# Performance work log

Measured on AMD Instinct MI355X. Metric: run time of the kernel, lower is better.

Reference implementation:

```python
import jax, jax.numpy as jnp
import numpy as np

N_NODES = 1024
NUM_MOL = 32
ATOMS = 32          # atoms per molecule
SDIM = 256
VDIM = 64
EDIM = 128
NUM_BOND_TYPES = 5


def _fully_connected_edges():
    # all ordered pairs (j, i), j != i, within each molecule block
    idx = np.arange(ATOMS)
    jj, ii = np.meshgrid(idx, idx, indexing='ij')
    mask = jj != ii
    jj, ii = jj[mask], ii[mask]                      # [ATOMS*(ATOMS-1)]
    offs = (np.arange(NUM_MOL) * ATOMS)[:, None]
    j_all = (jj[None, :] + offs).reshape(-1)
    i_all = (ii[None, :] + offs).reshape(-1)
    return np.stack([j_all, i_all]).astype(np.int32)  # [2, E]


def setup_inputs() -> dict:
    key = jax.random.key(0)
    ks = jax.random.split(key, 12)
    edge_index = jnp.asarray(_fully_connected_edges())  # [2, 31744]
    E = edge_index.shape[1]
    inp = {
        's': jax.random.normal(ks[0], (N_NODES, SDIM), jnp.float32),
        'v': jax.random.normal(ks[1], (N_NODES, 3, VDIM), jnp.float32),
        'p': jax.random.normal(ks[2], (N_NODES, 3), jnp.float32),
        'e': jax.random.normal(ks[3], (E, EDIM), jnp.float32),
        'batch': jnp.repeat(jnp.arange(NUM_MOL, dtype=jnp.int32), ATOMS),
        'edge_index': edge_index,
        # learned parameters
        'W_shared': jax.random.normal(ks[4], (SDIM, SDIM), jnp.float32) * 0.02,
        'b_shared': jnp.zeros((SDIM,), jnp.float32),
        'W_coords': jax.random.normal(ks[5], (VDIM, 1), jnp.float32) * 0.02,
        'W_bond': jax.random.normal(ks[6], (EDIM, SDIM), jnp.float32) * 0.02,
        'b_bond': jnp.zeros((SDIM,), jnp.float32),
        'W_b0': jax.random.normal(ks[7], (SDIM + 1, SDIM), jnp.float32) * 0.02,
        'b_b0': jnp.zeros((SDIM,), jnp.float32),
        'W_b1': jax.random.normal(ks[8], (SDIM, NUM_BOND_TYPES), jnp.float32) * 0.02,
        'b_b1': jnp.zeros((NUM_BOND_TYPES,), jnp.float32),
    }
    return inp


def reference(s, v, p, e, batch, edge_index,
              W_shared, b_shared, W_coords, W_bond, b_bond,
              W_b0, b_b0, W_b1, b_b1):
    n = s.shape[0]
    # shared_mapping: DenseLayer with SiLU
    s = jax.nn.silu(s @ W_shared + b_shared)
    # coords_lin: [n,3,vdim] @ [vdim,1] -> [n,3]
    coords = p + jnp.einsum('ncv,vo->nc', v, W_coords)
    # scatter_mean centering per molecule
    seg_sum = jax.ops.segment_sum(coords, batch, num_segments=NUM_MOL)
    counts = jax.ops.segment_sum(jnp.ones((n, 1), coords.dtype), batch,
                                 num_segments=NUM_MOL)
    mean = seg_sum / jnp.maximum(counts, 1.0)
    coords = coords - mean[batch]
    # dense symmetrization of edge features
    j, i = edge_index[0], edge_index[1]
    e_dense = jnp.zeros((n, n, e.shape[-1]), e.dtype).at[j, i].set(e)
    e_dense = 0.5 * (e_dense + jnp.swapaxes(e_dense, 0, 1))
    e_sym = e_dense[j, i]                                  # [E, EDIM]
    # squared distance per edge
    d = jnp.sum((coords[i] - coords[j]) ** 2, axis=-1, keepdims=True)  # [E,1]
    # edge MLP
    f = s[i] + s[j] + (e_sym @ W_bond + b_bond)            # [E, SDIM]
    edge = jnp.concatenate([f, d], axis=-1)                # [E, SDIM+1]
    h = jax.nn.silu(edge @ W_b0 + b_b0)
    bonds_pred = h @ W_b1 + b_b1                           # [E, 5]
    return bonds_pred
```

## Files before the change

### kernel.cpp

```cpp
#include <hip/hip_runtime.h>
#include <hip/hip_bf16.h>

#define N_NODES 1024
#define NUM_MOL 32
#define ATOMS 32
#define SDIM 256
#define VDIM 64
#define EDIM 128
#define NBT 5
#define EDGES_PER_MOL (ATOMS * (ATOMS - 1))
#define PAIRS_PER_MOL (ATOMS * (ATOMS - 1) / 2)
#define N_PAIRS (NUM_MOL * PAIRS_PER_MOL)

typedef __attribute__((ext_vector_type(8))) short bf16x8;
typedef __attribute__((ext_vector_type(4))) float f32x4;

__device__ __forceinline__ unsigned short f2bf(float x) {
    union { float f; unsigned int u; } v; v.f = x;
    unsigned int r = v.u + 0x7fffu + ((v.u >> 16) & 1u);
    return (unsigned short)(r >> 16);
}

__device__ __forceinline__ bf16x8 pack8(const float4& x0, const float4& x1) {
    bf16x8 r;
    r[0] = (short)f2bf(x0.x); r[1] = (short)f2bf(x0.y);
    r[2] = (short)f2bf(x0.z); r[3] = (short)f2bf(x0.w);
    r[4] = (short)f2bf(x1.x); r[5] = (short)f2bf(x1.y);
    r[6] = (short)f2bf(x1.z); r[7] = (short)f2bf(x1.w);
    return r;
}

__global__ __launch_bounds__(256) void prep_kernel(
    const float* __restrict__ Ws, const float* __restrict__ Wb0,
    unsigned short* __restrict__ Wsf, unsigned short* __restrict__ Wb0f)
{
    const int t   = threadIdx.x;
    const int bid = blockIdx.x;
    const float* W = (bid < 32) ? Ws : Wb0;
    unsigned short* dst = (bid < 32) ? Wsf : Wb0f;
    const int g    = ((bid & 31) << 8) + t;
    const int lane = g & 63;
    const int kt   = (g >> 6) & 7;
    const int nt   = g >> 9;
    const int n     = nt * 16 + (lane & 15);
    const int kbase = kt * 32 + (lane >> 4) * 8;
    const float* col = W + (size_t)kbase * SDIM + n;
    bf16x8 r;
#pragma unroll
    for (int e2 = 0; e2 < 8; ++e2) r[e2] = (short)f2bf(col[(size_t)e2 * SDIM]);
    *(bf16x8*)&dst[(size_t)g * 8] = r;
}

__global__ __launch_bounds__(256) void node_kernel(
    const float* __restrict__ s,
    const unsigned short* __restrict__ Wsf,
    const unsigned short* __restrict__ Wb0f,
    const float* __restrict__ bs,
    const float* __restrict__ Wbond, const float* __restrict__ bbond,
    const float* __restrict__ Wb0, const float* __restrict__ bb0,
    const float* __restrict__ v, const float* __restrict__ p,
    const float* __restrict__ Wc,
    float* __restrict__ sp2, unsigned short* __restrict__ Wf,
    float* __restrict__ coords, float* __restrict__ bcomb)
{
    __shared__ __align__(16) unsigned short s2u[16 * 256];
    const int t = threadIdx.x;
    const int bid = blockIdx.x;
    const int w = t >> 6, l = t & 63;
    const int kg = l >> 4, lr = l & 15;

    if (bid < 64) {
        const int r0 = bid * 16;

        bf16x8 a[8];
        const float* srow = s + (size_t)(r0 + lr) * SDIM + kg * 8;
#pragma unroll
        for (int kt = 0; kt < 8; ++kt) {
            const float4 x0 = *(const float4*)(srow + kt * 32);
            const float4 x1 = *(const float4*)(srow + kt * 32 + 4);
            a[kt] = pack8(x0, x1);
        }

        const bf16x8* wsp = (const bf16x8*)Wsf;
        f32x4 acc[4];
#pragma unroll
        for (int q = 0; q < 4; ++q) {
            acc[q][0] = 0.f; acc[q][1] = 0.f; acc[q][2] = 0.f; acc[q][3] = 0.f;
            const int nt = w * 4 + q;
#pragma unroll
            for (int kt = 0; kt < 8; ++kt) {
                const bf16x8 bf = wsp[(nt * 8 + kt) * 64 + l];
                acc[q] = __builtin_amdgcn_mfma_f32_16x16x32_bf16(a[kt], bf, acc[q], 0, 0, 0);
            }
        }

#pragma unroll
        for (int q = 0; q < 4; ++q) {
            const int n = (w * 4 + q) * 16 + lr;
            const float bsv = bs[n];
#pragma unroll
            for (int j = 0; j < 4; ++j) {
                const int row = kg * 4 + j;
                const float x = acc[q][j] + bsv;
                const float sl = x / (1.f + __expf(-x));
                s2u[(row * 256 + n) ^ ((row & 7) << 3)] = f2bf(sl);
            }
        }
        __syncthreads();

#pragma unroll
        for (int kt = 0; kt < 8; ++kt) {
            const int idx = (lr * 256 + kt * 32 + kg * 8) ^ ((lr & 7) << 3);
            a[kt] = *(const bf16x8*)&s2u[idx];
        }

        const bf16x8* wbp = (const bf16x8*)Wb0f;
#pragma unroll
        for (int q = 0; q < 4; ++q) {
            acc[q][0] = 0.f; acc[q][1] = 0.f; acc[q][2] = 0.f; acc[q][3] = 0.f;
            const int nt = w * 4 + q;
#pragma unroll
            for (int kt = 0; kt < 8; ++kt) {
                const bf16x8 bf = wbp[(nt * 8 + kt) * 64 + l];
                acc[q] = __builtin_amdgcn_mfma_f32_16x16x32_bf16(a[kt], bf, acc[q], 0, 0, 0);
            }
        }
#pragma unroll
        for (int q = 0; q < 4; ++q) {
            const int n = (w * 4 + q) * 16 + lr;
#pragma unroll
            for (int j = 0; j < 4; ++j)
                sp2[(size_t)(r0 + kg * 4 + j) * SDIM + n] = acc[q][j];
        }

    } else if (bid < 72) {
        const int r0 = (bid - 64) * 16;

        bf16x8 a[8];
        const float* wrow = Wbond + (size_t)(r0 + lr) * SDIM + kg * 8;
#pragma unroll
        for (int kt = 0; kt < 8; ++kt) {
            const float4 x0 = *(const float4*)(wrow + kt * 32);
            const float4 x1 = *(const float4*)(wrow + kt * 32 + 4);
            a[kt] = pack8(x0, x1);
        }

        const bf16x8* wbp = (const bf16x8*)Wb0f;
        f32x4 acc[4];
#pragma unroll
        for (int q = 0; q < 4; ++q) {
            acc[q][0] = 0.f; acc[q][1] = 0.f; acc[q][2] = 0.f; acc[q][3] = 0.f;
            const int nt = w * 4 + q;
#pragma unroll
            for (int kt = 0; kt < 8; ++kt) {
                const bf16x8 bf = wbp[(nt * 8 + kt) * 64 + l];
                acc[q] = __builtin_amdgcn_mfma_f32_16x16x32_bf16(a[kt], bf, acc[q], 0, 0, 0);
            }
        }

#pragma unroll
        for (int q = 0; q < 4; ++q) {
            const int nt2 = w * 4 + q;
#pragma unroll
            for (int j = 0; j < 4; ++j) {
                const int krow = r0 + kg * 4 + j;
                const int kt2 = krow >> 5, g2 = (krow >> 3) & 3, eidx = krow & 7;
                const int lane2 = lr + 16 * g2;
                Wf[((size_t)((nt2 * 4 + kt2) * 64 + lane2)) * 8 + eidx] =
                    f2bf(0.5f * acc[q][j]);
            }
        }

    } else if (bid < 104) {
        const int mol = bid - 72;
        float* cl   = (float*)s2u;
        float* mean = (float*)s2u + 100;
        if (t < ATOMS * 3) {
            const int a = t / 3, dim = t % 3;
            const int node = mol * ATOMS + a;
            const float* vv = v + (size_t)node * 3 * VDIM + dim * VDIM;
            float acc = 0.f;
#pragma unroll 8
            for (int k = 0; k < VDIM; ++k) acc += vv[k] * Wc[k];
            cl[a * 3 + dim] = p[node * 3 + dim] + acc;
        }
        __syncthreads();
        if (t < 3) {
            float sum = 0.f;
            for (int a = 0; a < ATOMS; ++a) sum += cl[a * 3 + t];
            mean[t] = sum * (1.f / ATOMS);
        }
        __syncthreads();
        if (t < ATOMS * 3) {
            const int a = t / 3, dim = t % 3;
            coords[(mol * ATOMS + a) * 3 + dim] = cl[a * 3 + dim] - mean[dim];
        }
    } else {
        float acc = bb0[t];
#pragma unroll 16
        for (int m = 0; m < SDIM; ++m) acc += bbond[m] * Wb0[m * SDIM + t];
        bcomb[t] = acc;
    }
}

#define PB 16
__global__ __launch_bounds__(256) void edge_mfma_kernel(
    const float* __restrict__ sp2, const float* __restrict__ coords,
    const float* __restrict__ e, const unsigned short* __restrict__ Wf,
    const float* __restrict__ bcomb, const float* __restrict__ Wb0,
    const float* __restrict__ Wb1, const float* __restrict__ bb1,
    float* __restrict__ out)
{
    __shared__ __align__(16) float spsum[PB][260];
    __shared__ __align__(16) unsigned short esym[PB * EDIM];
    __shared__ float wb1s[SDIM * NBT];
    __shared__ float bb1s[8];
    __shared__ int   ksh[PB], krevsh[PB], ish[PB], jsh[PB];
    __shared__ float dsh[PB];

    const int t = threadIdx.x;
    const int bid = (blockIdx.x & 7) * 124 + (blockIdx.x >> 3);
    const int P0  = bid * PB;

    for (int idx = t; idx < SDIM * NBT; idx += 256) wb1s[idx] = Wb1[idx];
    if (t < NBT) bb1s[t] = bb1[t];
    if (t < PB) {
        const int P   = P0 + t;
        const int mol = P / PAIRS_PER_MOL;
        const int p   = P - mol * PAIRS_PER_MOL;
        int jj = (int)((63.0f - sqrtf((float)(3969 - 8 * p))) * 0.5f);
        if (jj < 0) jj = 0;
        if (jj > 30) jj = 30;
        while (jj > 0 && (63 * jj - jj * jj) / 2 > p) --jj;
        while (jj < 30 && (63 * (jj + 1) - (jj + 1) * (jj + 1)) / 2 <= p) ++jj;
        const int Ojj = (63 * jj - jj * jj) / 2;
        const int ii  = jj + 1 + (p - Ojj);
        const int q    = jj * 31 + (ii - 1);
        const int qrev = ii * 31 + jj;
        ksh[t]    = mol * EDGES_PER_MOL + q;
        krevsh[t] = mol * EDGES_PER_MOL + qrev;
        const int i = mol * ATOMS + ii, j = mol * ATOMS + jj;
        ish[t] = i; jsh[t] = j;
        const float dx = coords[i * 3 + 0] - coords[j * 3 + 0];
        const float dy = coords[i * 3 + 1] - coords[j * 3 + 1];
        const float dz = coords[i * 3 + 2] - coords[j * 3 + 2];
        dsh[t] = dx * dx + dy * dy + dz * dz;
    }
    __syncthreads();

    {
        const int r  = t >> 4;
        const int c8 = (t & 15) * 8;
        const float* ek  = e + (size_t)ksh[r] * EDIM + c8;
        const float* ekr = e + (size_t)krevsh[r] * EDIM + c8;
        const float4 x0 = *(const float4*)(ek);
        const float4 x1 = *(const float4*)(ek + 4);
        const float4 y0 = *(const float4*)(ekr);
        const float4 y1 = *(const float4*)(ekr + 4);

        const int c0 = (t & 15) * 4;
        const float* ai = sp2 + (size_t)ish[r] * SDIM;
        const float* aj = sp2 + (size_t)jsh[r] * SDIM;
        const float* w2 = Wb0 + (size_t)SDIM * SDIM;
        const float d = dsh[r];
#pragma unroll
        for (int i = 0; i < 4; ++i) {
            const int c = c0 + 64 * i;
            const float4 a4 = *(const float4*)(ai + c);
            const float4 b4 = *(const float4*)(aj + c);
            const float4 w4 = *(const float4*)(w2 + c);
            const float4 g4 = *(const float4*)(bcomb + c);
            float4 rv;
            rv.x = a4.x + b4.x + d * w4.x + g4.x;
            rv.y = a4.y + b4.y + d * w4.y + g4.y;
            rv.z = a4.z + b4.z + d * w4.z + g4.z;
            rv.w = a4.w + b4.w + d * w4.w + g4.w;
            *(float4*)&spsum[r][c] = rv;
        }

        float4 sx, sy;
        sx.x = x0.x + y0.x; sx.y = x0.y + y0.y; sx.z = x0.z + y0.z; sx.w = x0.w + y0.w;
        sy.x = x1.x + y1.x; sy.y = x1.y + y1.y; sy.z = x1.z + y1.z; sy.w = x1.w + y1.w;
        const int idx = (r * EDIM + c8) ^ ((r & 7) << 3);
        *(bf16x8*)&esym[idx] = pack8(sx, sy);
    }
    __syncthreads();

    const int w = t >> 6, l = t & 63;
    const int kg = l >> 4, lr = l & 15;

    bf16x8 afrag[4];
#pragma unroll
    for (int kt = 0; kt < 4; ++kt) {
        const int idx = (lr * EDIM + kt * 32 + kg * 8) ^ ((lr & 7) << 3);
        afrag[kt] = *(const bf16x8*)&esym[idx];
    }

    const bf16x8* wfp = (const bf16x8*)Wf;
    f32x4 acc[4];
#pragma unroll
    for (int q = 0; q < 4; ++q) {
        acc[q][0] = 0.f; acc[q][1] = 0.f; acc[q][2] = 0.f; acc[q][3] = 0.f;
        const int nt = w * 4 + q;
        const bf16x8 b0 = wfp[(nt * 4 + 0) * 64 + l];
        const bf16x8 b1 = wfp[(nt * 4 + 1) * 64 + l];
        const bf16x8 b2 = wfp[(nt * 4 + 2) * 64 + l];
        const bf16x8 b3 = wfp[(nt * 4 + 3) * 64 + l];
        acc[q] = __builtin_amdgcn_mfma_f32_16x16x32_bf16(afrag[0], b0, acc[q], 0, 0, 0);
        acc[q] = __builtin_amdgcn_mfma_f32_16x16x32_bf16(afrag[1], b1, acc[q], 0, 0, 0);
        acc[q] = __builtin_amdgcn_mfma_f32_16x16x32_bf16(afrag[2], b2, acc[q], 0, 0, 0);
        acc[q] = __builtin_amdgcn_mfma_f32_16x16x32_bf16(afrag[3], b3, acc[q], 0, 0, 0);
    }

#pragma unroll
    for (int q = 0; q < 4; ++q) {
        const int n = (w * 4 + q) * 16 + lr;
#pragma unroll
        for (int j = 0; j < 4; ++j) {
            const int r = kg * 4 + j;
            const float x = acc[q][j] + spsum[r][n];
            spsum[r][n] = x / (1.f + __expf(-x));
        }
    }
    __syncthreads();

    if (t < PB * NBT * 2) {
        const int task = t >> 1, half = t & 1;
        const int r  = task / NBT;
        const int tt = task - r * NBT;
        float a = half ? 0.f : bb1s[tt];
        const int base = half * 32;
#pragma unroll 4
        for (int cc = 0; cc < 32; ++cc) {
            const int c4 = base + ((cc + task) & 31);
            const int c  = c4 * 4;
            const float4 hv = *(const float4*)&spsum[r][c];
            a += hv.x * wb1s[(c + 0) * NBT + tt] + hv.y * wb1s[(c + 1) * NBT + tt] +
                 hv.z * wb1s[(c + 2) * NBT + tt] + hv.w * wb1s[(c + 3) * NBT + tt];
        }
        a += __shfl_xor(a, 1);
        if (!half) {
            out[(size_t)ksh[r] * NBT + tt]    = a;
            out[(size_t)krevsh[r] * NBT + tt] = a;
        }
    }
}

extern "C" void kernel_launch(void* const* d_in, const int* in_sizes, int n_in,
                              void* d_out, int out_size, void* d_ws, size_t ws_size,
                              hipStream_t stream)
{
    const float* s        = (const float*)d_in[0];
    const float* v        = (const float*)d_in[1];
    const float* p        = (const float*)d_in[2];
    const float* e        = (const float*)d_in[3];
    const float* W_shared = (const float*)d_in[6];
    const float* b_shared = (const float*)d_in[7];
    const float* W_coords = (const float*)d_in[8];
    const float* W_bond   = (const float*)d_in[9];
    const float* b_bond   = (const float*)d_in[10];
    const float* W_b0     = (const float*)d_in[11];
    const float* b_b0     = (const float*)d_in[12];
    const float* W_b1     = (const float*)d_in[13];
    const float* b_b1     = (const float*)d_in[14];
    float* out = (float*)d_out;

    char* ws = (char*)d_ws;
    float*          sp2    = (float*)(ws + 0);
    unsigned short* Wsf    = (unsigned short*)(ws + 1048576);
    unsigned short* Wb0f   = (unsigned short*)(ws + 1179648);
    unsigned short* Wf     = (unsigned short*)(ws + 1310720);
    float*          bcomb  = (float*)(ws + 1376256);
    float*          coords = (float*)(ws + 1377280);

    prep_kernel<<<64, 256, 0, stream>>>(W_shared, W_b0, Wsf, Wb0f);
    node_kernel<<<105, 256, 0, stream>>>(s, Wsf, Wb0f, b_shared,
                                         W_bond, b_bond, W_b0, b_b0,
                                         v, p, W_coords,
                                         sp2, Wf, coords, bcomb);
    edge_mfma_kernel<<<N_PAIRS / PB, 256, 0, stream>>>(sp2, coords, e, Wf, bcomb,
                                                       W_b0, W_b1, b_b1, out);
}
```

Measured before the change: 28.12 us.

## Compute pair indices per thread, drop sync, prefetch MFMA weights before barrier

Every thread now computes its pair's edge indices and squared distance directly, so the first barrier and the serial 16-thread index stage are gone. The Wb1 staging is vectorised and moved after the gathers, and half of the bf16 weight fragments for the MFMA are prefetched into registers before the barrier to overlap global latency. The final projection loop gets two accumulators to shorten dependency chains. The cost is redundant index math in every thread and higher register pressure from the prefetched fragments.

```diff
diff --git a/kernel.cpp b/kernel.cpp
--- a/kernel.cpp
+++ b/kernel.cpp
@@ -213,59 +213,51 @@
 {
     __shared__ __align__(16) float spsum[PB][260];
     __shared__ __align__(16) unsigned short esym[PB * EDIM];
-    __shared__ float wb1s[SDIM * NBT];
+    __shared__ __align__(16) float wb1s[SDIM * NBT];
     __shared__ float bb1s[8];
-    __shared__ int   ksh[PB], krevsh[PB], ish[PB], jsh[PB];
-    __shared__ float dsh[PB];
+    __shared__ int   ksh[PB], krevsh[PB];
 
     const int t = threadIdx.x;
     const int bid = (blockIdx.x & 7) * 124 + (blockIdx.x >> 3);
     const int P0  = bid * PB;
 
-    for (int idx = t; idx < SDIM * NBT; idx += 256) wb1s[idx] = Wb1[idx];
-    if (t < NBT) bb1s[t] = bb1[t];
-    if (t < PB) {
-        const int P   = P0 + t;
-        const int mol = P / PAIRS_PER_MOL;
-        const int p   = P - mol * PAIRS_PER_MOL;
-        int jj = (int)((63.0f - sqrtf((float)(3969 - 8 * p))) * 0.5f);
-        if (jj < 0) jj = 0;
-        if (jj > 30) jj = 30;
-        while (jj > 0 && (63 * jj - jj * jj) / 2 > p) --jj;
-        while (jj < 30 && (63 * (jj + 1) - (jj + 1) * (jj + 1)) / 2 <= p) ++jj;
-        const int Ojj = (63 * jj - jj * jj) / 2;
-        const int ii  = jj + 1 + (p - Ojj);
-        const int q    = jj * 31 + (ii - 1);
-        const int qrev = ii * 31 + jj;
-        ksh[t]    = mol * EDGES_PER_MOL + q;
-        krevsh[t] = mol * EDGES_PER_MOL + qrev;
-        const int i = mol * ATOMS + ii, j = mol * ATOMS + jj;
-        ish[t] = i; jsh[t] = j;
-        const float dx = coords[i * 3 + 0] - coords[j * 3 + 0];
-        const float dy = coords[i * 3 + 1] - coords[j * 3 + 1];
-        const float dz = coords[i * 3 + 2] - coords[j * 3 + 2];
-        dsh[t] = dx * dx + dy * dy + dz * dz;
-    }
-    __syncthreads();
+    const int r   = t >> 4;
+    const int P   = P0 + r;
+    const int mol = P / PAIRS_PER_MOL;
+    const int p   = P - mol * PAIRS_PER_MOL;
+    int jj = (int)((63.0f - sqrtf((float)(3969 - 8 * p))) * 0.5f);
+    if (jj < 0) jj = 0;
+    if (jj > 30) jj = 30;
+    while (jj > 0 && (63 * jj - jj * jj) / 2 > p) --jj;
+    while (jj < 30 && (63 * (jj + 1) - (jj + 1) * (jj + 1)) / 2 <= p) ++jj;
+    const int Ojj  = (63 * jj - jj * jj) / 2;
+    const int ii   = jj + 1 + (p - Ojj);
+    const int k    = mol * EDGES_PER_MOL + jj * 31 + (ii - 1);
+    const int krev = mol * EDGES_PER_MOL + ii * 31 + jj;
+    const int i = mol * ATOMS + ii, j = mol * ATOMS + jj;
+    if ((t & 15) == 0) { ksh[r] = k; krevsh[r] = krev; }
+
+    const int c8 = (t & 15) * 8;
+    const float* ek  = e + (size_t)k * EDIM + c8;
+    const float* ekr = e + (size_t)krev * EDIM + c8;
+    const float4 x0 = *(const float4*)(ek);
+    const float4 x1 = *(const float4*)(ek + 4);
+    const float4 y0 = *(const float4*)(ekr);
+    const float4 y1 = *(const float4*)(ekr + 4);
+
+    const float dx = coords[i * 3 + 0] - coords[j * 3 + 0];
+    const float dy = coords[i * 3 + 1] - coords[j * 3 + 1];
+    const float dz = coords[i * 3 + 2] - coords[j * 3 + 2];
+    const float d  = dx * dx + dy * dy + dz * dz;
 
     {
-        const int r  = t >> 4;
-        const int c8 = (t & 15) * 8;
-        const float* ek  = e + (size_t)ksh[r] * EDIM + c8;
-        const float* ekr = e + (size_t)krevsh[r] * EDIM + c8;
-        const float4 x0 = *(const float4*)(ek);
-        const float4 x1 = *(const float4*)(ek + 4);
-        const float4 y0 = *(const float4*)(ekr);
-        const float4 y1 = *(const float4*)(ekr + 4);
-
         const int c0 = (t & 15) * 4;
-        const float* ai = sp2 + (size_t)ish[r] * SDIM;
-        const float* aj = sp2 + (size_t)jsh[r] * SDIM;
+        const float* ai = sp2 + (size_t)i * SDIM;
+        const float* aj = sp2 + (size_t)j * SDIM;
         const float* w2 = Wb0 + (size_t)SDIM * SDIM;
-        const float d = dsh[r];
-#pragma unroll
-        for (int i = 0; i < 4; ++i) {
-            const int c = c0 + 64 * i;
+#pragma unroll
+        for (int it = 0; it < 4; ++it) {
+            const int c = c0 + 64 * it;
             const float4 a4 = *(const float4*)(ai + c);
             const float4 b4 = *(const float4*)(aj + c);
             const float4 w4 = *(const float4*)(w2 + c);
@@ -277,17 +269,31 @@
             rv.w = a4.w + b4.w + d * w4.w + g4.w;
             *(float4*)&spsum[r][c] = rv;
         }
-
+    }
+
+    {
         float4 sx, sy;
         sx.x = x0.x + y0.x; sx.y = x0.y + y0.y; sx.z = x0.z + y0.z; sx.w = x0.w + y0.w;
         sy.x = x1.x + y1.x; sy.y = x1.y + y1.y; sy.z = x1.z + y1.z; sy.w = x1.w + y1.w;
         const int idx = (r * EDIM + c8) ^ ((r & 7) << 3);
         *(bf16x8*)&esym[idx] = pack8(sx, sy);
     }
-    __syncthreads();
+
+    for (int idx4 = t; idx4 < SDIM * NBT / 4; idx4 += 256)
+        *(float4*)&wb1s[idx4 * 4] = *(const float4*)&Wb1[idx4 * 4];
+    if (t < NBT) bb1s[t] = bb1[t];
 
     const int w = t >> 6, l = t & 63;
     const int kg = l >> 4, lr = l & 15;
+    const bf16x8* wfp = (const bf16x8*)Wf;
+    bf16x8 bpre[8];
+#pragma unroll
+    for (int q = 0; q < 2; ++q)
+#pragma unroll
+        for (int kt = 0; kt < 4; ++kt)
+            bpre[q * 4 + kt] = wfp[((w * 4 + q) * 4 + kt) * 64 + l];
+
+    __syncthreads();
 
     bf16x8 afrag[4];
 #pragma unroll
@@ -296,10 +302,17 @@
         afrag[kt] = *(const bf16x8*)&esym[idx];
     }
 
-    const bf16x8* wfp = (const bf16x8*)Wf;
     f32x4 acc[4];
 #pragma unroll
-    for (int q = 0; q < 4; ++q) {
+    for (int q = 0; q < 2; ++q) {
+        acc[q][0] = 0.f; acc[q][1] = 0.f; acc[q][2] = 0.f; acc[q][3] = 0.f;
+        acc[q] = __builtin_amdgcn_mfma_f32_16x16x32_bf16(afrag[0], bpre[q * 4 + 0], acc[q], 0, 0, 0);
+        acc[q] = __builtin_amdgcn_mfma_f32_16x16x32_bf16(afrag[1], bpre[q * 4 + 1], acc[q], 0, 0, 0);
+        acc[q] = __builtin_amdgcn_mfma_f32_16x16x32_bf16(afrag[2], bpre[q * 4 + 2], acc[q], 0, 0, 0);
+        acc[q] = __builtin_amdgcn_mfma_f32_16x16x32_bf16(afrag[3], bpre[q * 4 + 3], acc[q], 0, 0, 0);
+    }
+#pragma unroll
+    for (int q = 2; q < 4; ++q) {
         acc[q][0] = 0.f; acc[q][1] = 0.f; acc[q][2] = 0.f; acc[q][3] = 0.f;
         const int nt = w * 4 + q;
         const bf16x8 b0 = wfp[(nt * 4 + 0) * 64 + l];
@@ -316,32 +329,37 @@
     for (int q = 0; q < 4; ++q) {
         const int n = (w * 4 + q) * 16 + lr;
 #pragma unroll
-        for (int j = 0; j < 4; ++j) {
-            const int r = kg * 4 + j;
-            const float x = acc[q][j] + spsum[r][n];
-            spsum[r][n] = x / (1.f + __expf(-x));
+        for (int jt = 0; jt < 4; ++jt) {
+            const int rr = kg * 4 + jt;
+            const float x = acc[q][jt] + spsum[rr][n];
+            spsum[rr][n] = x / (1.f + __expf(-x));
         }
     }
     __syncthreads();
 
     if (t < PB * NBT * 2) {
         const int task = t >> 1, half = t & 1;
-        const int r  = task / NBT;
-        const int tt = task - r * NBT;
-        float a = half ? 0.f : bb1s[tt];
+        const int rr = task / NBT;
+        const int tt = task - rr * NBT;
+        float a0 = half ? 0.f : bb1s[tt];
+        float a1 = 0.f;
         const int base = half * 32;
 #pragma unroll 4
-        for (int cc = 0; cc < 32; ++cc) {
-            const int c4 = base + ((cc + task) & 31);
-            const int c  = c4 * 4;
-            const float4 hv = *(const float4*)&spsum[r][c];
-            a += hv.x * wb1s[(c + 0) * NBT + tt] + hv.y * wb1s[(c + 1) * NBT + tt] +
-                 hv.z * wb1s[(c + 2) * NBT + tt] + hv.w * wb1s[(c + 3) * NBT + tt];
-        }
+        for (int cc = 0; cc < 32; cc += 2) {
+            const int ca = (base + ((cc + task) & 31)) * 4;
+            const int cb = (base + ((cc + 1 + task) & 31)) * 4;
+            const float4 hva = *(const float4*)&spsum[rr][ca];
+            const float4 hvb = *(const float4*)&spsum[rr][cb];
+            a0 += hva.x * wb1s[(ca + 0) * NBT + tt] + hva.y * wb1s[(ca + 1) * NBT + tt] +
+                  hva.z * wb1s[(ca + 2) * NBT + tt] + hva.w * wb1s[(ca + 3) * NBT + tt];
+            a1 += hvb.x * wb1s[(cb + 0) * NBT + tt] + hvb.y * wb1s[(cb + 1) * NBT + tt] +
+                  hvb.z * wb1s[(cb + 2) * NBT + tt] + hvb.w * wb1s[(cb + 3) * NBT + tt];
+        }
+        float a = a0 + a1;
         a += __shfl_xor(a, 1);
         if (!half) {
-            out[(size_t)ksh[r] * NBT + tt]    = a;
-            out[(size_t)krevsh[r] * NBT + tt] = a;
+            out[(size_t)ksh[rr] * NBT + tt]    = a;
+            out[(size_t)krevsh[rr] * NBT + tt] = a;
         }
     }
 }
```

After: 28.66 us. No clear change (+2.0%).

## Fuse weight prep into node kernel via LDS-staged fp32 weight chunks

Applied to the files above, without the earlier changes.

Drops the separate prep kernel that converted W_shared and W_b0 into MFMA-swizzled bf16 layouts. Each GEMM block now streams 32-row fp32 chunks of the weight into LDS with register double-buffering, then converts to bf16 per lane while reading the B operand. This saves one kernel launch and the extra global round trip for the packed weights. In exchange every block re-reads and re-converts the full weight matrices, adds many barriers, and uses more LDS.

```diff
diff --git a/kernel.cpp b/kernel.cpp
--- a/kernel.cpp
+++ b/kernel.cpp
@@ -30,32 +30,16 @@
     return r;
 }
 
-__global__ __launch_bounds__(256) void prep_kernel(
-    const float* __restrict__ Ws, const float* __restrict__ Wb0,
-    unsigned short* __restrict__ Wsf, unsigned short* __restrict__ Wb0f)
-{
-    const int t   = threadIdx.x;
-    const int bid = blockIdx.x;
-    const float* W = (bid < 32) ? Ws : Wb0;
-    unsigned short* dst = (bid < 32) ? Wsf : Wb0f;
-    const int g    = ((bid & 31) << 8) + t;
-    const int lane = g & 63;
-    const int kt   = (g >> 6) & 7;
-    const int nt   = g >> 9;
-    const int n     = nt * 16 + (lane & 15);
-    const int kbase = kt * 32 + (lane >> 4) * 8;
-    const float* col = W + (size_t)kbase * SDIM + n;
-    bf16x8 r;
-#pragma unroll
-    for (int e2 = 0; e2 < 8; ++e2) r[e2] = (short)f2bf(col[(size_t)e2 * SDIM]);
-    *(bf16x8*)&dst[(size_t)g * 8] = r;
-}
-
-__global__ __launch_bounds__(256) void node_kernel(
+#define CHS 258
+
+struct PreSm {
+    float chunk[32][CHS];
+    unsigned short s2u[16 * 256];
+};
+
+__global__ __launch_bounds__(256) void pre_kernel(
     const float* __restrict__ s,
-    const unsigned short* __restrict__ Wsf,
-    const unsigned short* __restrict__ Wb0f,
-    const float* __restrict__ bs,
+    const float* __restrict__ Ws, const float* __restrict__ bs,
     const float* __restrict__ Wbond, const float* __restrict__ bbond,
     const float* __restrict__ Wb0, const float* __restrict__ bb0,
     const float* __restrict__ v, const float* __restrict__ p,
@@ -63,35 +47,81 @@
     float* __restrict__ sp2, unsigned short* __restrict__ Wf,
     float* __restrict__ coords, float* __restrict__ bcomb)
 {
-    __shared__ __align__(16) unsigned short s2u[16 * 256];
+    __shared__ __align__(16) char smem[sizeof(PreSm)];
+    PreSm* sm = (PreSm*)smem;
     const int t = threadIdx.x;
     const int bid = blockIdx.x;
     const int w = t >> 6, l = t & 63;
     const int kg = l >> 4, lr = l & 15;
 
-    if (bid < 64) {
-        const int r0 = bid * 16;
+    if (bid < 72) {
+        const bool isnode = (bid < 64);
+        const int r0 = isnode ? bid * 16 : (bid - 64) * 16;
 
         bf16x8 a[8];
-        const float* srow = s + (size_t)(r0 + lr) * SDIM + kg * 8;
+        {
+            const float* arow = (isnode ? s : Wbond) + (size_t)(r0 + lr) * SDIM + kg * 8;
+#pragma unroll
+            for (int kt = 0; kt < 8; ++kt) {
+                const float4 x0 = *(const float4*)(arow + kt * 32);
+                const float4 x1 = *(const float4*)(arow + kt * 32 + 4);
+                a[kt] = pack8(x0, x1);
+            }
+        }
+
+        f32x4 acc[4];
+        float4 stg[8];
+        const float* Wg1 = isnode ? Ws : Wb0;
+
+#pragma unroll
+        for (int i = 0; i < 8; ++i) {
+            const int idx = t + 256 * i, row = idx >> 6, c4 = idx & 63;
+            stg[i] = *(const float4*)&Wg1[(size_t)row * SDIM + c4 * 4];
+        }
+#pragma unroll
+        for (int q = 0; q < 4; ++q) { acc[q][0]=0.f; acc[q][1]=0.f; acc[q][2]=0.f; acc[q][3]=0.f; }
+
 #pragma unroll
         for (int kt = 0; kt < 8; ++kt) {
-            const float4 x0 = *(const float4*)(srow + kt * 32);
-            const float4 x1 = *(const float4*)(srow + kt * 32 + 4);
-            a[kt] = pack8(x0, x1);
-        }
-
-        const bf16x8* wsp = (const bf16x8*)Wsf;
-        f32x4 acc[4];
-#pragma unroll
-        for (int q = 0; q < 4; ++q) {
-            acc[q][0] = 0.f; acc[q][1] = 0.f; acc[q][2] = 0.f; acc[q][3] = 0.f;
-            const int nt = w * 4 + q;
-#pragma unroll
-            for (int kt = 0; kt < 8; ++kt) {
-                const bf16x8 bf = wsp[(nt * 8 + kt) * 64 + l];
+#pragma unroll
+            for (int i = 0; i < 8; ++i) {
+                const int idx = t + 256 * i, row = idx >> 6, c4 = idx & 63;
+                *(float4*)&sm->chunk[row][c4 * 4] = stg[i];
+            }
+            __syncthreads();
+            if (kt < 7) {
+                const float* wsrc = Wg1 + (size_t)((kt + 1) * 32) * SDIM;
+#pragma unroll
+                for (int i = 0; i < 8; ++i) {
+                    const int idx = t + 256 * i, row = idx >> 6, c4 = idx & 63;
+                    stg[i] = *(const float4*)&wsrc[(size_t)row * SDIM + c4 * 4];
+                }
+            }
+#pragma unroll
+            for (int q = 0; q < 4; ++q) {
+                const int n = (w * 4 + q) * 16 + lr;
+                bf16x8 bf;
+#pragma unroll
+                for (int e2 = 0; e2 < 8; ++e2) bf[e2] = (short)f2bf(sm->chunk[kg * 8 + e2][n]);
                 acc[q] = __builtin_amdgcn_mfma_f32_16x16x32_bf16(a[kt], bf, acc[q], 0, 0, 0);
             }
+            __syncthreads();
+        }
+
+        if (!isnode) {
+#pragma unroll
+            for (int q = 0; q < 4; ++q) {
+                const int nt2 = w * 4 + q;
+#pragma unroll
+                for (int j = 0; j < 4; ++j) {
+                    const int krow = r0 + kg * 4 + j;
+                    const int kt2 = krow >> 5, g2 = (krow >> 3) & 3, eidx = krow & 7;
+                    const int lane2 = lr + 16 * g2;
+                    Wf[((size_t)((nt2 * 4 + kt2) * 64 + lane2)) * 8 + eidx] =
+                        f2bf(0.5f * acc[q][j]);
+                }
+            }
+            return;
         }
 
 #pragma unroll
@@ -103,7 +133,7 @@
                 const int row = kg * 4 + j;
                 const float x = acc[q][j] + bsv;
                 const float sl = x / (1.f + __expf(-x));
-                s2u[(row * 256 + n) ^ ((row & 7) << 3)] = f2bf(sl);
+                sm->s2u[(row * 256 + n) ^ ((row & 7) << 3)] = f2bf(sl);
             }
         }
         __syncthreads();
@@ -111,17 +141,40 @@
 #pragma unroll
         for (int kt = 0; kt < 8; ++kt) {
             const int idx = (lr * 256 + kt * 32 + kg * 8) ^ ((lr & 7) << 3);
-            a[kt] = *(const bf16x8*)&s2u[idx];
-        }
-
-        const bf16x8* wbp = (const bf16x8*)Wb0f;
-#pragma unroll
-        for (int q = 0; q < 4; ++q) {
-            acc[q][0] = 0.f; acc[q][1] = 0.f; acc[q][2] = 0.f; acc[q][3] = 0.f;
-            const int nt = w * 4 + q;
-#pragma unroll
-            for (int kt = 0; kt < 8; ++kt) {
-                const bf16x8 bf = wbp[(nt * 8 + kt) * 64 + l];
+            a[kt] = *(const bf16x8*)&sm->s2u[idx];
+        }
+
+#pragma unroll
+        for (int i = 0; i < 8; ++i) {
+            const int idx = t + 256 * i, row = idx >> 6, c4 = idx & 63;
+            stg[i] = *(const float4*)&Wb0[(size_t)row * SDIM + c4 * 4];
+        }
+#pragma unroll
+        for (int q = 0; q < 4; ++q) { acc[q][0]=0.f; acc[q][1]=0.f; acc[q][2]=0.f; acc[q][3]=0.f; }
+
+#pragma unroll
+        for (int kt = 0; kt < 8; ++kt) {
+            __syncthreads();
+#pragma unroll
+            for (int i = 0; i < 8; ++i) {
+                const int idx = t + 256 * i, row = idx >> 6, c4 = idx & 63;
+                *(float4*)&sm->chunk[row][c4 * 4] = stg[i];
+            }
+            __syncthreads();
+            if (kt < 7) {
+                const float* wsrc = Wb0 + (size_t)((kt + 1) * 32) * SDIM;
+#pragma unroll
+                for (int i = 0; i < 8; ++i) {
+                    const int idx = t + 256 * i, row = idx >> 6, c4 = idx & 63;
+                    stg[i] = *(const float4*)&wsrc[(size_t)row * SDIM + c4 * 4];
+                }
+            }
+#pragma unroll
+            for (int q = 0; q < 4; ++q) {
+                const int n = (w * 4 + q) * 16 + lr;
+                bf16x8 bf;
+#pragma unroll
+                for (int e2 = 0; e2 < 8; ++e2) bf[e2] = (short)f2bf(sm->chunk[kg * 8 + e2][n]);
                 acc[q] = __builtin_amdgcn_mfma_f32_16x16x32_bf16(a[kt], bf, acc[q], 0, 0, 0);
             }
         }
@@ -133,67 +186,29 @@
                 sp2[(size_t)(r0 + kg * 4 + j) * SDIM + n] = acc[q][j];
         }
 
-    } else if (bid < 72) {
-        const int r0 = (bid - 64) * 16;
-
-        bf16x8 a[8];
-        const float* wrow = Wbond + (size_t)(r0 + lr) * SDIM + kg * 8;
-#pragma unroll
-        for (int kt = 0; kt < 8; ++kt) {
-            const float4 x0 = *(const float4*)(wrow + kt * 32);
-            const float4 x1 = *(const float4*)(wrow + kt * 32 + 4);
-            a[kt] = pack8(x0, x1);
-        }
-
-        const bf16x8* wbp = (const bf16x8*)Wb0f;
-        f32x4 acc[4];
-#pragma unroll
-        for (int q = 0; q < 4; ++q) {
-            acc[q][0] = 0.f; acc[q][1] = 0.f; acc[q][2] = 0.f; acc[q][3] = 0.f;
-            const int nt = w * 4 + q;
-#pragma unroll
-            for (int kt = 0; kt < 8; ++kt) {
-                const bf16x8 bf = wbp[(nt * 8 + kt) * 64 + l];
-                acc[q] = __builtin_amdgcn_mfma_f32_16x16x32_bf16(a[kt], bf, acc[q], 0, 0, 0);
-            }
-        }
-
-#pragma unroll
-        for (int q = 0; q < 4; ++q) {
-            const int nt2 = w * 4 + q;
-#pragma unroll
-            for (int j = 0; j < 4; ++j) {
-                const int krow = r0 + kg * 4 + j;
-                const int kt2 = krow >> 5, g2 = (krow >> 3) & 3, eidx = krow & 7;
-                const int lane2 = lr + 16 * g2;
-                Wf[((size_t)((nt2 * 4 + kt2) * 64 + lane2)) * 8 + eidx] =
-                    f2bf(0.5f * acc[q][j]);
-            }
-        }
-
     } else if (bid < 104) {
         const int mol = bid - 72;
-        float* cl   = (float*)s2u;
-        float* mean = (float*)s2u + 100;
+        float* cl   = (float*)smem;
+        float* mean = (float*)smem + 100;
         if (t < ATOMS * 3) {
-            const int a = t / 3, dim = t % 3;
-            const int node = mol * ATOMS + a;
+            const int a2 = t / 3, dim = t % 3;
+            const int node = mol * ATOMS + a2;
             const float* vv = v + (size_t)node * 3 * VDIM + dim * VDIM;
             float acc = 0.f;
 #pragma unroll 8
-            for (int k = 0; k < VDIM; ++k) acc += vv[k] * Wc[k];
-            cl[a * 3 + dim] = p[node * 3 + dim] + acc;
+            for (int k2 = 0; k2 < VDIM; ++k2) acc += vv[k2] * Wc[k2];
+            cl[a2 * 3 + dim] = p[node * 3 + dim] + acc;
         }
         __syncthreads();
         if (t < 3) {
             float sum = 0.f;
-            for (int a = 0; a < ATOMS; ++a) sum += cl[a * 3 + t];
+            for (int a2 = 0; a2 < ATOMS; ++a2) sum += cl[a2 * 3 + t];
             mean[t] = sum * (1.f / ATOMS);
         }
         __syncthreads();
         if (t < ATOMS * 3) {
-            const int a = t / 3, dim = t % 3;
-            coords[(mol * ATOMS + a) * 3 + dim] = cl[a * 3 + dim] - mean[dim];
+            const int a2 = t / 3, dim = t % 3;
+            coords[(mol * ATOMS + a2) * 3 + dim] = cl[a2 * 3 + dim] - mean[dim];
         }
     } else {
         float acc = bb0[t];
@@ -367,17 +382,14 @@
 
     char* ws = (char*)d_ws;
     float*          sp2    = (float*)(ws + 0);
-    unsigned short* Wsf    = (unsigned short*)(ws + 1048576);
-    unsigned short* Wb0f   = (unsigned short*)(ws + 1179648);
-    unsigned short* Wf     = (unsigned short*)(ws + 1310720);
-    float*          bcomb  = (float*)(ws + 1376256);
-    float*          coords = (float*)(ws + 1377280);
-
-    prep_kernel<<<64, 256, 0, stream>>>(W_shared, W_b0, Wsf, Wb0f);
-    node_kernel<<<105, 256, 0, stream>>>(s, Wsf, Wb0f, b_shared,
-                                         W_bond, b_bond, W_b0, b_b0,
-                                         v, p, W_coords,
-                                         sp2, Wf, coords, bcomb);
+    unsigned short* Wf     = (unsigned short*)(ws + 1048576);
+    float*          bcomb  = (float*)(ws + 1114112);
+    float*          coords = (float*)(ws + 1115136);
+
+    pre_kernel<<<105, 256, 0, stream>>>(s, W_shared, b_shared,
+                                        W_bond, b_bond, W_b0, b_b0,
+                                        v, p, W_coords,
+                                        sp2, Wf, coords, bcomb);
     edge_mfma_kernel<<<N_PAIRS / PB, 256, 0, stream>>>(sp2, coords, e, Wf, bcomb,
                                                        W_b0, W_b1, b_b1, out);
 }
```

Result: slower. 62.86 us (+123.6%).
